# Kernel optimization log

Measured on AMD Instinct MI355X. Metric: run time of the kernel, lower is better.

Reference implementation:

```python
import jax, jax.numpy as jnp
import numpy as np

MAX_SCALE = 4
EPS = 1e-7        # tf.keras.backend.epsilon()
BN_EPS = 1e-3     # Keras BatchNormalization default epsilon


def setup_inputs() -> dict:
    key = jax.random.key(0)
    k1, = jax.random.split(key, 1)
    B, H, W, C = 16, 224, 224, 32
    x = jax.random.uniform(k1, (B, H, W, C), dtype=jnp.float32)
    gamma = jnp.ones((C,), jnp.float32)
    beta = jnp.zeros((C,), jnp.float32)
    moving_mean = jnp.zeros((C,), jnp.float32)
    moving_var = jnp.ones((C,), jnp.float32)
    return {"x": x, "gamma": gamma, "beta": beta,
            "moving_mean": moving_mean, "moving_var": moving_var}


def _box_sum(x, r):
    # Depthwise conv with an all-ones (r, r) kernel, SAME padding (NHWC).
    # reduce_window SAME padding matches TF conv SAME for stride 1.
    return jax.lax.reduce_window(x, 0.0, jax.lax.add,
                                 window_dimensions=(1, r, r, 1),
                                 window_strides=(1, 1, 1, 1),
                                 padding="SAME")


def reference(x, gamma, beta, moving_mean, moving_var):
    # sample_min_max_scaling: per-sample min-max over H, W, C
    mn = jnp.min(x, axis=(1, 2, 3), keepdims=True)
    mx = jnp.max(x, axis=(1, 2, 3), keepdims=True)
    xs = (x - mn) / (mx - mn + EPS)

    scales = [2 ** i for i in range(1, MAX_SCALE + 1)]  # [2,4,8,16]
    # measures: [B, H, W, C, S]
    measures = jnp.stack([_box_sum(xs, r) for r in scales], axis=-1)

    # OLS slope of log(measure) vs log(scale), per pixel/channel
    log_scales = jnp.log(jnp.asarray(scales, jnp.float32))        # [S]
    log_measures = jnp.log(measures + EPS)                         # [B,H,W,C,S]
    ls_c = log_scales - jnp.mean(log_scales)                       # centered [S]
    lm_c = log_measures - jnp.mean(log_measures, axis=-1, keepdims=True)
    alphas = jnp.sum(lm_c * ls_c, axis=-1) / jnp.sum(ls_c ** 2)    # [B,H,W,C]

    # BatchNorm, inference mode (training=False)
    inv = jax.lax.rsqrt(moving_var + BN_EPS)
    return (alphas - moving_mean) * inv * gamma + beta
```

## Files before the change

kernel.cpp:

```cpp
#include <hip/hip_runtime.h>
#include <cstdint>

#define B_ 16
#define H_ 224
#define W_ 224
#define C_ 32
#define HW_ (H_*W_)

__device__ __forceinline__ unsigned int enc_f32(float f) {
    unsigned int u = __float_as_uint(f);
    return (u & 0x80000000u) ? ~u : (u | 0x80000000u);
}
__device__ __forceinline__ float dec_f32(unsigned int u) {
    unsigned int v = (u & 0x80000000u) ? (u & 0x7fffffffu) : ~u;
    return __uint_as_float(v);
}

__global__ void k_init(unsigned int* scratch) {
    int t = threadIdx.x;
    if (t < B_) { scratch[t] = 0xFFFFFFFFu; scratch[B_ + t] = 0u; }
}

__global__ __launch_bounds__(256) void k_minmax(
        const float* __restrict__ x, unsigned int* __restrict__ scratch) {
    __shared__ float rmin[4], rmax[4];
    int t = threadIdx.x;
    int b = blockIdx.y;
    const float4* p = (const float4*)(x + (size_t)b * HW_ * C_);
    const int n4 = HW_ * C_ / 4;
    float vmin = 1e30f, vmax = -1e30f;
    for (int i = blockIdx.x * 256 + t; i < n4; i += gridDim.x * 256) {
        float4 v = p[i];
        vmin = fminf(vmin, fminf(fminf(v.x, v.y), fminf(v.z, v.w)));
        vmax = fmaxf(vmax, fmaxf(fmaxf(v.x, v.y), fmaxf(v.z, v.w)));
    }
    for (int off = 32; off; off >>= 1) {
        vmin = fminf(vmin, __shfl_down(vmin, off));
        vmax = fmaxf(vmax, __shfl_down(vmax, off));
    }
    if ((t & 63) == 0) { rmin[t >> 6] = vmin; rmax[t >> 6] = vmax; }
    __syncthreads();
    if (t == 0) {
        atomicMin(&scratch[b],      enc_f32(fminf(fminf(rmin[0], rmin[1]), fminf(rmin[2], rmin[3]))));
        atomicMax(&scratch[B_ + b], enc_f32(fmaxf(fmaxf(rmax[0], rmax[1]), fmaxf(rmax[2], rmax[3]))));
    }
}

__global__ __launch_bounds__(512, 4) void k_fused(
        const float* __restrict__ x, float* __restrict__ out,
        const float* __restrict__ gamma, const float* __restrict__ beta,
        const float* __restrict__ mmean, const float* __restrict__ mvar,
        const unsigned int* __restrict__ scratch) {
    __shared__ float lin[2][8][132];
    __shared__ float lout[2][8][132];
    const int t    = threadIdx.x;
    const int wid  = t >> 6;
    const int lane = t & 63;

    int bid   = blockIdx.x;
    int cg    = bid & 3;
    int strip = (bid >> 2) & 1;
    int chunk = (bid >> 3) & 3;
    int b     = bid >> 5;

    const int c     = cg * 8 + wid;
    const int cbase = cg * 8;
    const int h0    = chunk * 56;
    const int sbase = strip * 112;

    float sc = gamma[c] * rsqrtf(mvar[c] + 1e-3f);
    float bi = beta[c] - mmean[c] * sc;

    float mn   = dec_f32(scratch[b]);
    float mx   = dec_f32(scratch[B_ + b]);
    float inv  = 1.0f / (mx - mn + 1e-7f);
    float minv = mn * inv;

    int c0 = sbase - 8 + 2 * lane;
    int c1 = c0 + 1;
    bool mC = (c0 >= 0) && (c0 <= W_ - 2);

    int col_l = t >> 2;
    int lch   = (t & 3) * 2;
    int wld   = min(max(sbase - 8 + col_l, 0), W_ - 1);
    int wst   = sbase - 8 + col_l;
    bool colok = (col_l >= 8) && (col_l < 120);
    const float* xb = x   + (size_t)b * HW_ * C_ + cbase + lch;
    float*       ob = out + (size_t)b * HW_ * C_ + cbase + lch;

    float cw2_0  = (float)(min(c0+1, W_-1) - c0 + 1);
    float cw2_1  = (float)(min(c1+1, W_-1) - c1 + 1);
    float cw4_0  = (float)(min(c0+2, W_-1) - max(c0-1, 0) + 1);
    float cw4_1  = (float)(min(c1+2, W_-1) - max(c1-1, 0) + 1);
    float cw8_0  = (float)(min(c0+4, W_-1) - max(c0-3, 0) + 1);
    float cw8_1  = (float)(min(c1+4, W_-1) - max(c1-3, 0) + 1);
    float cw16_0 = (float)(min(c0+8, W_-1) - max(c0-7, 0) + 1);
    float cw16_1 = (float)(min(c1+8, W_-1) - max(c1-7, 0) + 1);
    float e2_0  = minv * cw2_0,  e2_1  = minv * cw2_1;
    float e4_0  = minv * cw4_0,  e4_1  = minv * cw4_1;
    float e8_0  = minv * cw8_0,  e8_1  = minv * cw8_1;
    float e16_0 = minv * cw16_0, e16_1 = minv * cw16_1;
    float d2_0  = 1e-7f -  2.0f * e2_0,  d2_1  = 1e-7f -  2.0f * e2_1;
    float d4_0  = 1e-7f -  4.0f * e4_0,  d4_1  = 1e-7f -  4.0f * e4_1;
    float d8_0  = 1e-7f -  8.0f * e8_0,  d8_1  = 1e-7f -  8.0f * e8_1;
    float d16_0 = 1e-7f - 16.0f * e16_0, d16_1 = 1e-7f - 16.0f * e16_1;

    float hp0 = 0.f, hp1 = 0.f;
    float rB4[2][2]  = {};
    float rB8[2][4]  = {};
    float rB16[2][8] = {};
    float acc[2][8]  = {};

#define LDROW(AR) (*(const float2*)(xb + (size_t)((min(max((AR), 0), H_-1)) * W_ + wld) * C_))

    float2 q0, q1;
    {
        float2 qi = LDROW(h0 - 7);
        lin[1][lch][col_l]     = qi.x;
        lin[1][lch + 1][col_l] = qi.y;
        q0 = LDROW(h0 - 6);
        q1 = LDROW(h0 - 5);
    }

    for (int g8 = 0; g8 < 9; ++g8) {
        #pragma unroll
        for (int u = 0; u < 8; ++u) {
            int it = g8 * 8 + u;
            int a  = h0 - 7 + it;
            __syncthreads();
            float2 lv = *(const float2*)&lin[(u + 1) & 1][wid][2 * lane];
            lin[u & 1][lch][col_l]     = q0.x;
            lin[u & 1][lch + 1][col_l] = q0.y;
            q0 = q1;
            q1 = LDROW(a + 3);
            if (it >= 16 && colok) {
                int op = h0 - 16 + it;
                float2 sv;
                sv.x = lout[u & 1][lch][col_l];
                sv.y = lout[u & 1][lch + 1][col_l];
                *(float2*)(ob + (size_t)(op * W_ + wst) * C_) = sv;
            }

            bool rowok = (a >= 0) && (a < H_);
            float x0 = (rowok && mC) ? lv.x : 0.f;
            float x1 = (rowok && mC) ? lv.y : 0.f;
            float nx0 = __shfl_down(x0, 1);
            float xh0 = x0 + x1;
            float xh1 = x1 + nx0;
            float g2_0 = hp0 + xh0; hp0 = xh0;
            float g2_1 = hp1 + xh1; hp1 = xh1;
            float b4n_0 = g2_0 + __shfl_down(g2_0, 1);
            float b4n_1 = g2_1 + __shfl_down(g2_1, 1);
            float a4_0 = rB4[0][u & 1] + b4n_0; rB4[0][u & 1] = b4n_0;
            float a4_1 = rB4[1][u & 1] + b4n_1; rB4[1][u & 1] = b4n_1;
            float b8n_0 = a4_0 + __shfl_down(a4_0, 2);
            float b8n_1 = a4_1 + __shfl_down(a4_1, 2);
            float a8_0 = rB8[0][u & 3] + b8n_0; rB8[0][u & 3] = b8n_0;
            float a8_1 = rB8[1][u & 3] + b8n_1; rB8[1][u & 3] = b8n_1;
            float b16n_0 = a8_0 + __shfl_down(a8_0, 4);
            float b16n_1 = a8_1 + __shfl_down(a8_1, 4);
            float a16_0 = rB16[0][u] + b16n_0; rB16[0][u] = b16n_0;
            float a16_1 = rB16[1][u] + b16n_1; rB16[1][u] = b16n_1;
            float g4_0  = __shfl_up(a4_1, 1);
            float g4_1  = a4_0;
            float g8_0  = __shfl_up(a8_1, 2);
            float g8_1  = __shfl_up(a8_0, 1);
            float g16_0 = __shfl_up(a16_1, 4);
            float g16_1 = __shfl_up(a16_0, 3);

            float l1_0, l1_1, l2_0, l2_1, l3_0, l3_1, l4_0, l4_1;
            if (a >= 15 && a <= 223) {
                l1_0 = __log2f(fmaxf(fmaf(g2_0,  inv, d2_0 ), 1e-7f));
                l1_1 = __log2f(fmaxf(fmaf(g2_1,  inv, d2_1 ), 1e-7f));
                l2_0 = __log2f(fmaxf(fmaf(g4_0,  inv, d4_0 ), 1e-7f));
                l2_1 = __log2f(fmaxf(fmaf(g4_1,  inv, d4_1 ), 1e-7f));
                l3_0 = __log2f(fmaxf(fmaf(g8_0,  inv, d8_0 ), 1e-7f));
                l3_1 = __log2f(fmaxf(fmaf(g8_1,  inv, d8_1 ), 1e-7f));
                l4_0 = __log2f(fmaxf(fmaf(g16_0, inv, d16_0), 1e-7f));
                l4_1 = __log2f(fmaxf(fmaf(g16_1, inv, d16_1), 1e-7f));
            } else {
                int o1 = a - 1, o2 = a - 2, o3 = a - 4, o4 = a - 8;
                float ch2  = (float)(min(o1+1, H_-1) - o1 + 1);
                float ch4  = (float)(min(o2+2, H_-1) - max(o2-1, 0) + 1);
                float ch8  = (float)(min(o3+4, H_-1) - max(o3-3, 0) + 1);
                float ch16 = (float)(min(o4+8, H_-1) - max(o4-7, 0) + 1);
                l1_0 = __log2f(fmaxf(fmaf(-e2_0,  ch2,  fmaf(g2_0,  inv, 1e-7f)), 1e-7f));
                l1_1 = __log2f(fmaxf(fmaf(-e2_1,  ch2,  fmaf(g2_1,  inv, 1e-7f)), 1e-7f));
                l2_0 = __log2f(fmaxf(fmaf(-e4_0,  ch4,  fmaf(g4_0,  inv, 1e-7f)), 1e-7f));
                l2_1 = __log2f(fmaxf(fmaf(-e4_1,  ch4,  fmaf(g4_1,  inv, 1e-7f)), 1e-7f));
                l3_0 = __log2f(fmaxf(fmaf(-e8_0,  ch8,  fmaf(g8_0,  inv, 1e-7f)), 1e-7f));
                l3_1 = __log2f(fmaxf(fmaf(-e8_1,  ch8,  fmaf(g8_1,  inv, 1e-7f)), 1e-7f));
                l4_0 = __log2f(fmaxf(fmaf(-e16_0, ch16, fmaf(g16_0, inv, 1e-7f)), 1e-7f));
                l4_1 = __log2f(fmaxf(fmaf(-e16_1, ch16, fmaf(g16_1, inv, 1e-7f)), 1e-7f));
            }
            acc[0][u] = -0.3f * l1_0;
            acc[1][u] = -0.3f * l1_1;
            acc[0][(u+7)&7] = fmaf(-0.1f, l2_0, acc[0][(u+7)&7]);
            acc[1][(u+7)&7] = fmaf(-0.1f, l2_1, acc[1][(u+7)&7]);
            acc[0][(u+5)&7] = fmaf( 0.1f, l3_0, acc[0][(u+5)&7]);
            acc[1][(u+5)&7] = fmaf( 0.1f, l3_1, acc[1][(u+5)&7]);
            if (it >= 15 && it <= 70) {
                float al0 = fmaf(0.3f, l4_0, acc[0][(u+1)&7]);
                float al1 = fmaf(0.3f, l4_1, acc[1][(u+1)&7]);
                float2 ev;
                ev.x = fmaf(sc, al0, bi);
                ev.y = fmaf(sc, al1, bi);
                *(float2*)&lout[(u + 1) & 1][wid][2 * lane] = ev;
            }
        }
    }
#undef LDROW
}

extern "C" void kernel_launch(void* const* d_in, const int* in_sizes, int n_in,
                              void* d_out, int out_size, void* d_ws, size_t ws_size,
                              hipStream_t stream) {
    const float* x     = (const float*)d_in[0];
    const float* gamma = (const float*)d_in[1];
    const float* beta  = (const float*)d_in[2];
    const float* mmean = (const float*)d_in[3];
    const float* mvar  = (const float*)d_in[4];
    float* out = (float*)d_out;

    unsigned int* scratch = (unsigned int*)d_ws;

    k_init<<<1, 64, 0, stream>>>(scratch);
    k_minmax<<<dim3(128, B_), 256, 0, stream>>>(x, scratch);
    k_fused<<<512, 512, 0, stream>>>(x, out, gamma, beta, mmean, mvar, scratch);
}
```

Measured before the change: 308.9 us.

## Process all 32 channels per block with 4 channels per wave and shorter row chunks

Each block now covers all 32 channels of a strip (4 channels per wave) rather than an 8-channel group, so each pixel is read with full 128-byte coalesced float4 loads. To keep the grid size manageable, rows are split into 7 chunks of 32 instead of 4 chunks of 56, and the grid is cut from 512 to 224 blocks. The output buffer is single-buffered, with an extra barrier added per row, and occupancy drops to 2 blocks per CU because per-thread register state grows fourfold. The 16-row halo now makes up a larger share of each shorter chunk, and 224 blocks may underfill the GPU's compute units.

```diff
diff --git a/kernel.cpp b/kernel.cpp
--- a/kernel.cpp
+++ b/kernel.cpp
@@ -46,30 +46,34 @@
     }
 }
 
-__global__ __launch_bounds__(512, 4) void k_fused(
+__global__ __launch_bounds__(512, 2) void k_fused(
         const float* __restrict__ x, float* __restrict__ out,
         const float* __restrict__ gamma, const float* __restrict__ beta,
         const float* __restrict__ mmean, const float* __restrict__ mvar,
         const unsigned int* __restrict__ scratch) {
-    __shared__ float lin[2][8][132];
-    __shared__ float lout[2][8][132];
+    __shared__ float lin[2][32][134];
+    __shared__ float lout[32][134];
     const int t    = threadIdx.x;
     const int wid  = t >> 6;
     const int lane = t & 63;
 
     int bid   = blockIdx.x;
-    int cg    = bid & 3;
-    int strip = (bid >> 2) & 1;
-    int chunk = (bid >> 3) & 3;
-    int b     = bid >> 5;
-
-    const int c     = cg * 8 + wid;
-    const int cbase = cg * 8;
-    const int h0    = chunk * 56;
+    int chunk = bid % 7;
+    int bs    = bid / 7;
+    int strip = bs & 1;
+    int b     = bs >> 1;
+
+    const int cch   = wid * 4;
+    const int h0    = chunk * 32;
     const int sbase = strip * 112;
 
-    float sc = gamma[c] * rsqrtf(mvar[c] + 1e-3f);
-    float bi = beta[c] - mmean[c] * sc;
+    float sc[4], bi[4];
+    #pragma unroll
+    for (int k = 0; k < 4; ++k) {
+        float s = gamma[cch + k] * rsqrtf(mvar[cch + k] + 1e-3f);
+        sc[k] = s;
+        bi[k] = beta[cch + k] - mmean[cch + k] * s;
+    }
 
     float mn   = dec_f32(scratch[b]);
     float mx   = dec_f32(scratch[B_ + b]);
@@ -80,13 +84,13 @@
     int c1 = c0 + 1;
     bool mC = (c0 >= 0) && (c0 <= W_ - 2);
 
-    int col_l = t >> 2;
-    int lch   = (t & 3) * 2;
-    int wld   = min(max(sbase - 8 + col_l, 0), W_ - 1);
-    int wst   = sbase - 8 + col_l;
-    bool colok = (col_l >= 8) && (col_l < 120);
-    const float* xb = x   + (size_t)b * HW_ * C_ + cbase + lch;
-    float*       ob = out + (size_t)b * HW_ * C_ + cbase + lch;
+    int p    = t >> 2;
+    int chb  = (t & 3) * 8;
+    int gw   = min(max(sbase - 8 + p, 0), W_ - 1);
+    int gws  = sbase - 8 + p;
+    bool colok = (p >= 8) && (p < 120);
+    const float* xb = x   + (size_t)b * HW_ * C_ + chb;
+    float*       ob = out + (size_t)b * HW_ * C_ + chb;
 
     float cw2_0  = (float)(min(c0+1, W_-1) - c0 + 1);
     float cw2_1  = (float)(min(c1+1, W_-1) - c1 + 1);
@@ -105,111 +109,132 @@
     float d8_0  = 1e-7f -  8.0f * e8_0,  d8_1  = 1e-7f -  8.0f * e8_1;
     float d16_0 = 1e-7f - 16.0f * e16_0, d16_1 = 1e-7f - 16.0f * e16_1;
 
-    float hp0 = 0.f, hp1 = 0.f;
-    float rB4[2][2]  = {};
-    float rB8[2][4]  = {};
-    float rB16[2][8] = {};
-    float acc[2][8]  = {};
-
-#define LDROW(AR) (*(const float2*)(xb + (size_t)((min(max((AR), 0), H_-1)) * W_ + wld) * C_))
-
-    float2 q0, q1;
+    float hp0[4] = {}, hp1[4] = {};
+    float rB4[4][2][2]  = {};
+    float rB8[4][2][4]  = {};
+    float rB16[4][2][8] = {};
+    float acc[4][2][8]  = {};
+
+#define LDR(DA, DB, AR) { int r_ = min(max((AR), 0), H_-1); \
+    const float* rp_ = xb + ((size_t)r_ * W_ + gw) * C_; \
+    DA = *(const float4*)rp_; DB = *(const float4*)(rp_ + 4); }
+
+    float4 q0a, q0b;
     {
-        float2 qi = LDROW(h0 - 7);
-        lin[1][lch][col_l]     = qi.x;
-        lin[1][lch + 1][col_l] = qi.y;
-        q0 = LDROW(h0 - 6);
-        q1 = LDROW(h0 - 5);
-    }
-
-    for (int g8 = 0; g8 < 9; ++g8) {
+        float4 ta, tb;
+        LDR(ta, tb, h0 - 7);
+        lin[1][chb+0][p] = ta.x; lin[1][chb+1][p] = ta.y;
+        lin[1][chb+2][p] = ta.z; lin[1][chb+3][p] = ta.w;
+        lin[1][chb+4][p] = tb.x; lin[1][chb+5][p] = tb.y;
+        lin[1][chb+6][p] = tb.z; lin[1][chb+7][p] = tb.w;
+        LDR(q0a, q0b, h0 - 6);
+    }
+
+    for (int g8 = 0; g8 < 6; ++g8) {
         #pragma unroll
         for (int u = 0; u < 8; ++u) {
             int it = g8 * 8 + u;
             int a  = h0 - 7 + it;
             __syncthreads();
-            float2 lv = *(const float2*)&lin[(u + 1) & 1][wid][2 * lane];
-            lin[u & 1][lch][col_l]     = q0.x;
-            lin[u & 1][lch + 1][col_l] = q0.y;
-            q0 = q1;
-            q1 = LDROW(a + 3);
+            float2 lv[4];
+            #pragma unroll
+            for (int k = 0; k < 4; ++k)
+                lv[k] = *(const float2*)&lin[(u + 1) & 1][cch + k][2 * lane];
+            lin[u & 1][chb+0][p] = q0a.x; lin[u & 1][chb+1][p] = q0a.y;
+            lin[u & 1][chb+2][p] = q0a.z; lin[u & 1][chb+3][p] = q0a.w;
+            lin[u & 1][chb+4][p] = q0b.x; lin[u & 1][chb+5][p] = q0b.y;
+            lin[u & 1][chb+6][p] = q0b.z; lin[u & 1][chb+7][p] = q0b.w;
+            LDR(q0a, q0b, a + 2);
             if (it >= 16 && colok) {
                 int op = h0 - 16 + it;
-                float2 sv;
-                sv.x = lout[u & 1][lch][col_l];
-                sv.y = lout[u & 1][lch + 1][col_l];
-                *(float2*)(ob + (size_t)(op * W_ + wst) * C_) = sv;
+                float4 sa, sb;
+                sa.x = lout[chb+0][p]; sa.y = lout[chb+1][p];
+                sa.z = lout[chb+2][p]; sa.w = lout[chb+3][p];
+                sb.x = lout[chb+4][p]; sb.y = lout[chb+5][p];
+                sb.z = lout[chb+6][p]; sb.w = lout[chb+7][p];
+                float* wp = ob + ((size_t)op * W_ + gws) * C_;
+                *(float4*)wp = sa; *(float4*)(wp + 4) = sb;
             }
+            __syncthreads();
 
             bool rowok = (a >= 0) && (a < H_);
-            float x0 = (rowok && mC) ? lv.x : 0.f;
-            float x1 = (rowok && mC) ? lv.y : 0.f;
-            float nx0 = __shfl_down(x0, 1);
-            float xh0 = x0 + x1;
-            float xh1 = x1 + nx0;
-            float g2_0 = hp0 + xh0; hp0 = xh0;
-            float g2_1 = hp1 + xh1; hp1 = xh1;
-            float b4n_0 = g2_0 + __shfl_down(g2_0, 1);
-            float b4n_1 = g2_1 + __shfl_down(g2_1, 1);
-            float a4_0 = rB4[0][u & 1] + b4n_0; rB4[0][u & 1] = b4n_0;
-            float a4_1 = rB4[1][u & 1] + b4n_1; rB4[1][u & 1] = b4n_1;
-            float b8n_0 = a4_0 + __shfl_down(a4_0, 2);
-            float b8n_1 = a4_1 + __shfl_down(a4_1, 2);
-            float a8_0 = rB8[0][u & 3] + b8n_0; rB8[0][u & 3] = b8n_0;
-            float a8_1 = rB8[1][u & 3] + b8n_1; rB8[1][u & 3] = b8n_1;
-            float b16n_0 = a8_0 + __shfl_down(a8_0, 4);
-            float b16n_1 = a8_1 + __shfl_down(a8_1, 4);
-            float a16_0 = rB16[0][u] + b16n_0; rB16[0][u] = b16n_0;
-            float a16_1 = rB16[1][u] + b16n_1; rB16[1][u] = b16n_1;
-            float g4_0  = __shfl_up(a4_1, 1);
-            float g4_1  = a4_0;
-            float g8_0  = __shfl_up(a8_1, 2);
-            float g8_1  = __shfl_up(a8_0, 1);
-            float g16_0 = __shfl_up(a16_1, 4);
-            float g16_1 = __shfl_up(a16_0, 3);
-
-            float l1_0, l1_1, l2_0, l2_1, l3_0, l3_1, l4_0, l4_1;
-            if (a >= 15 && a <= 223) {
-                l1_0 = __log2f(fmaxf(fmaf(g2_0,  inv, d2_0 ), 1e-7f));
-                l1_1 = __log2f(fmaxf(fmaf(g2_1,  inv, d2_1 ), 1e-7f));
-                l2_0 = __log2f(fmaxf(fmaf(g4_0,  inv, d4_0 ), 1e-7f));
-                l2_1 = __log2f(fmaxf(fmaf(g4_1,  inv, d4_1 ), 1e-7f));
-                l3_0 = __log2f(fmaxf(fmaf(g8_0,  inv, d8_0 ), 1e-7f));
-                l3_1 = __log2f(fmaxf(fmaf(g8_1,  inv, d8_1 ), 1e-7f));
-                l4_0 = __log2f(fmaxf(fmaf(g16_0, inv, d16_0), 1e-7f));
-                l4_1 = __log2f(fmaxf(fmaf(g16_1, inv, d16_1), 1e-7f));
-            } else {
+            bool interior = (a >= 15) && (a <= 223);
+            float ch2 = 0.f, ch4 = 0.f, ch8 = 0.f, ch16 = 0.f;
+            if (!interior) {
                 int o1 = a - 1, o2 = a - 2, o3 = a - 4, o4 = a - 8;
-                float ch2  = (float)(min(o1+1, H_-1) - o1 + 1);
-                float ch4  = (float)(min(o2+2, H_-1) - max(o2-1, 0) + 1);
-                float ch8  = (float)(min(o3+4, H_-1) - max(o3-3, 0) + 1);
-                float ch16 = (float)(min(o4+8, H_-1) - max(o4-7, 0) + 1);
-                l1_0 = __log2f(fmaxf(fmaf(-e2_0,  ch2,  fmaf(g2_0,  inv, 1e-7f)), 1e-7f));
-                l1_1 = __log2f(fmaxf(fmaf(-e2_1,  ch2,  fmaf(g2_1,  inv, 1e-7f)), 1e-7f));
-                l2_0 = __log2f(fmaxf(fmaf(-e4_0,  ch4,  fmaf(g4_0,  inv, 1e-7f)), 1e-7f));
-                l2_1 = __log2f(fmaxf(fmaf(-e4_1,  ch4,  fmaf(g4_1,  inv, 1e-7f)), 1e-7f));
-                l3_0 = __log2f(fmaxf(fmaf(-e8_0,  ch8,  fmaf(g8_0,  inv, 1e-7f)), 1e-7f));
-                l3_1 = __log2f(fmaxf(fmaf(-e8_1,  ch8,  fmaf(g8_1,  inv, 1e-7f)), 1e-7f));
-                l4_0 = __log2f(fmaxf(fmaf(-e16_0, ch16, fmaf(g16_0, inv, 1e-7f)), 1e-7f));
-                l4_1 = __log2f(fmaxf(fmaf(-e16_1, ch16, fmaf(g16_1, inv, 1e-7f)), 1e-7f));
+                ch2  = (float)(min(o1+1, H_-1) - o1 + 1);
+                ch4  = (float)(min(o2+2, H_-1) - max(o2-1, 0) + 1);
+                ch8  = (float)(min(o3+4, H_-1) - max(o3-3, 0) + 1);
+                ch16 = (float)(min(o4+8, H_-1) - max(o4-7, 0) + 1);
             }
-            acc[0][u] = -0.3f * l1_0;
-            acc[1][u] = -0.3f * l1_1;
-            acc[0][(u+7)&7] = fmaf(-0.1f, l2_0, acc[0][(u+7)&7]);
-            acc[1][(u+7)&7] = fmaf(-0.1f, l2_1, acc[1][(u+7)&7]);
-            acc[0][(u+5)&7] = fmaf( 0.1f, l3_0, acc[0][(u+5)&7]);
-            acc[1][(u+5)&7] = fmaf( 0.1f, l3_1, acc[1][(u+5)&7]);
-            if (it >= 15 && it <= 70) {
-                float al0 = fmaf(0.3f, l4_0, acc[0][(u+1)&7]);
-                float al1 = fmaf(0.3f, l4_1, acc[1][(u+1)&7]);
-                float2 ev;
-                ev.x = fmaf(sc, al0, bi);
-                ev.y = fmaf(sc, al1, bi);
-                *(float2*)&lout[(u + 1) & 1][wid][2 * lane] = ev;
+            bool doemit = (it >= 15 && it <= 46);
+
+            #pragma unroll
+            for (int k = 0; k < 4; ++k) {
+                float x0 = (rowok && mC) ? lv[k].x : 0.f;
+                float x1 = (rowok && mC) ? lv[k].y : 0.f;
+                float nx0 = __shfl_down(x0, 1);
+                float xh0 = x0 + x1;
+                float xh1 = x1 + nx0;
+                float g2_0 = hp0[k] + xh0; hp0[k] = xh0;
+                float g2_1 = hp1[k] + xh1; hp1[k] = xh1;
+                float b4n_0 = g2_0 + __shfl_down(g2_0, 1);
+                float b4n_1 = g2_1 + __shfl_down(g2_1, 1);
+                float a4_0 = rB4[k][0][u & 1] + b4n_0; rB4[k][0][u & 1] = b4n_0;
+                float a4_1 = rB4[k][1][u & 1] + b4n_1; rB4[k][1][u & 1] = b4n_1;
+                float b8n_0 = a4_0 + __shfl_down(a4_0, 2);
+                float b8n_1 = a4_1 + __shfl_down(a4_1, 2);
+                float a8_0 = rB8[k][0][u & 3] + b8n_0; rB8[k][0][u & 3] = b8n_0;
+                float a8_1 = rB8[k][1][u & 3] + b8n_1; rB8[k][1][u & 3] = b8n_1;
+                float b16n_0 = a8_0 + __shfl_down(a8_0, 4);
+                float b16n_1 = a8_1 + __shfl_down(a8_1, 4);
+                float a16_0 = rB16[k][0][u] + b16n_0; rB16[k][0][u] = b16n_0;
+                float a16_1 = rB16[k][1][u] + b16n_1; rB16[k][1][u] = b16n_1;
+                float g4_0  = __shfl_up(a4_1, 1);
+                float g4_1  = a4_0;
+                float g8_0  = __shfl_up(a8_1, 2);
+                float g8_1  = __shfl_up(a8_0, 1);
+                float g16_0 = __shfl_up(a16_1, 4);
+                float g16_1 = __shfl_up(a16_0, 3);
+
+                float l1_0, l1_1, l2_0, l2_1, l3_0, l3_1, l4_0, l4_1;
+                if (interior) {
+                    l1_0 = __log2f(fmaxf(fmaf(g2_0,  inv, d2_0 ), 1e-7f));
+                    l1_1 = __log2f(fmaxf(fmaf(g2_1,  inv, d2_1 ), 1e-7f));
+                    l2_0 = __log2f(fmaxf(fmaf(g4_0,  inv, d4_0 ), 1e-7f));
+                    l2_1 = __log2f(fmaxf(fmaf(g4_1,  inv, d4_1 ), 1e-7f));
+                    l3_0 = __log2f(fmaxf(fmaf(g8_0,  inv, d8_0 ), 1e-7f));
+                    l3_1 = __log2f(fmaxf(fmaf(g8_1,  inv, d8_1 ), 1e-7f));
+                    l4_0 = __log2f(fmaxf(fmaf(g16_0, inv, d16_0), 1e-7f));
+                    l4_1 = __log2f(fmaxf(fmaf(g16_1, inv, d16_1), 1e-7f));
+                } else {
+                    l1_0 = __log2f(fmaxf(fmaf(-e2_0,  ch2,  fmaf(g2_0,  inv, 1e-7f)), 1e-7f));
+                    l1_1 = __log2f(fmaxf(fmaf(-e2_1,  ch2,  fmaf(g2_1,  inv, 1e-7f)), 1e-7f));
+                    l2_0 = __log2f(fmaxf(fmaf(-e4_0,  ch4,  fmaf(g4_0,  inv, 1e-7f)), 1e-7f));
+                    l2_1 = __log2f(fmaxf(fmaf(-e4_1,  ch4,  fmaf(g4_1,  inv, 1e-7f)), 1e-7f));
+                    l3_0 = __log2f(fmaxf(fmaf(-e8_0,  ch8,  fmaf(g8_0,  inv, 1e-7f)), 1e-7f));
+                    l3_1 = __log2f(fmaxf(fmaf(-e8_1,  ch8,  fmaf(g8_1,  inv, 1e-7f)), 1e-7f));
+                    l4_0 = __log2f(fmaxf(fmaf(-e16_0, ch16, fmaf(g16_0, inv, 1e-7f)), 1e-7f));
+                    l4_1 = __log2f(fmaxf(fmaf(-e16_1, ch16, fmaf(g16_1, inv, 1e-7f)), 1e-7f));
+                }
+                acc[k][0][u] = -0.3f * l1_0;
+                acc[k][1][u] = -0.3f * l1_1;
+                acc[k][0][(u+7)&7] = fmaf(-0.1f, l2_0, acc[k][0][(u+7)&7]);
+                acc[k][1][(u+7)&7] = fmaf(-0.1f, l2_1, acc[k][1][(u+7)&7]);
+                acc[k][0][(u+5)&7] = fmaf( 0.1f, l3_0, acc[k][0][(u+5)&7]);
+                acc[k][1][(u+5)&7] = fmaf( 0.1f, l3_1, acc[k][1][(u+5)&7]);
+                if (doemit) {
+                    float al0 = fmaf(0.3f, l4_0, acc[k][0][(u+1)&7]);
+                    float al1 = fmaf(0.3f, l4_1, acc[k][1][(u+1)&7]);
+                    float2 ev;
+                    ev.x = fmaf(sc[k], al0, bi[k]);
+                    ev.y = fmaf(sc[k], al1, bi[k]);
+                    *(float2*)&lout[cch + k][2 * lane] = ev;
+                }
             }
         }
     }
-#undef LDROW
+#undef LDR
 }
 
 extern "C" void kernel_launch(void* const* d_in, const int* in_sizes, int n_in,
@@ -226,5 +251,5 @@
 
     k_init<<<1, 64, 0, stream>>>(scratch);
     k_minmax<<<dim3(128, B_), 256, 0, stream>>>(x, scratch);
-    k_fused<<<512, 512, 0, stream>>>(x, out, gamma, beta, mmean, mvar, scratch);
-}
+    k_fused<<<224, 512, 0, stream>>>(x, out, gamma, beta, mmean, mvar, scratch);
+}
```

After: 435.8 us. +41.1%, slower.
